# Optimization experiments

Measured on AMD Instinct MI355X. Metric: run time of the kernel, lower is better.

## Reference

```python
import jax, jax.numpy as jnp
import numpy as np

B, N, P = 8, 4096, 1024
P4 = P // 4
EPS = 1e-5


def _ln(x, g, b):
    mu = jnp.mean(x, axis=-1, keepdims=True)
    var = jnp.var(x, axis=-1, keepdims=True)
    return (x - mu) * jax.lax.rsqrt(var + EPS) * g + b


def setup_inputs() -> dict:
    key = jax.random.key(0)
    ks = jax.random.split(key, 16)
    s = lambda fan: 1.0 / np.sqrt(fan)
    return {
        "xyz": jax.random.normal(ks[0], (B, N, 3), jnp.float32),
        "x": jax.random.normal(ks[1], (B, N, P), jnp.float32),
        "ln1_g": jnp.ones((P,), jnp.float32),
        "ln1_b": jnp.zeros((P,), jnp.float32),
        "ln2_g": jnp.ones((P,), jnp.float32),
        "ln2_b": jnp.zeros((P,), jnp.float32),
        "qk_w": jax.random.normal(ks[2], (P4, P), jnp.float32) * s(P),   # shared q/k 1x1 conv, no bias
        "v_w": jax.random.normal(ks[3], (P, P), jnp.float32) * s(P),
        "v_b": jax.random.normal(ks[4], (P,), jnp.float32) * s(P),
        "t1_w": jax.random.normal(ks[5], (P, P4), jnp.float32) * s(P4),  # trans_conv
        "t1_b": jax.random.normal(ks[6], (P,), jnp.float32) * s(P4),
        "t2_w": jax.random.normal(ks[7], (P, P4), jnp.float32) * s(P4),  # trans_conv1
        "t2_b": jax.random.normal(ks[8], (P,), jnp.float32) * s(P4),
        "m1_w": jax.random.normal(ks[9], (P, P), jnp.float32) * s(P),
        "m1_b": jax.random.normal(ks[10], (P,), jnp.float32) * s(P),
        "m2_w": jax.random.normal(ks[11], (P, P), jnp.float32) * s(P),
        "m2_b": jax.random.normal(ks[12], (P,), jnp.float32) * s(P),
    }


def reference(xyz, x, ln1_g, ln1_b, ln2_g, ln2_b, qk_w, v_w, v_b,
              t1_w, t1_b, t2_w, t2_b, m1_w, m1_b, m2_w, m2_b):
    # xyz is accepted but unused, matching the torch module. Dropout = eval identity.
    res1 = x
    h = _ln(x, ln1_g, ln1_b)                                   # [B,N,P]
    # TransformerBlock_1 (1x1 convs on h^T [B,P,N] are just matmuls over P)
    x_q = jnp.einsum('op,bnp->bon', qk_w, h)                   # [B,P4,N]
    # k shares weights with q; x_k permuted is x_q transposed
    x_v = jnp.einsum('op,bnp->bno', v_w, h) + v_b              # [B,N,P]
    energy = jnp.einsum('bqn,bkn->bqk', x_q, x_q)              # [B,P4,P4]
    att = jnp.einsum('op,bpk->bok', t1_w, energy) + t1_b[:, None]   # [B,P,P4]
    att = jax.nn.gelu(att, approximate=False)
    att = jnp.einsum('op,bkp->bok', t2_w, att) + t2_b[:, None]      # [B,P,P]
    att = jax.nn.softmax(att, axis=-1)
    t_out = jnp.einsum('bnp,bpq->bnq', x_v, att)               # [B,N,P]
    x1 = t_out + res1
    h2 = _ln(x1, ln2_g, ln2_b)
    m = jax.nn.gelu(h2 @ m1_w.T + m1_b, approximate=False)
    m = m @ m2_w.T + m2_b
    return x1 + m
```

## Files before the change

kernel.cpp:

```cpp
#include <hip/hip_runtime.h>


typedef __attribute__((ext_vector_type(4))) float f32x4;
typedef __attribute__((ext_vector_type(8))) _Float16 h16x8;
typedef __attribute__((ext_vector_type(8))) unsigned short u16x8;
typedef __attribute__((ext_vector_type(4))) unsigned short u16x4;

__device__ __forceinline__ unsigned short f2h(float f) {
  _Float16 h = (_Float16)f;
  return __builtin_bit_cast(unsigned short, h);
}
__device__ __forceinline__ unsigned split16(float f) {
  _Float16 h = (_Float16)f;
  _Float16 l = (_Float16)(f - (float)h);
  return (unsigned)__builtin_bit_cast(unsigned short, h) |
         ((unsigned)__builtin_bit_cast(unsigned short, l) << 16);
}
__device__ __forceinline__ float gelu_f(float x) {
  return 0.5f * x * (1.0f + erff(x * 0.70710678118654752f));
}
__device__ __forceinline__ void gload16(const void* g, void* l) {
  __builtin_amdgcn_global_load_lds(
      (const __attribute__((address_space(1))) unsigned int*)g,
      (__attribute__((address_space(3))) unsigned int*)l, 16, 0, 0);
}
#define FENCE() asm volatile("" ::: "memory")

__global__ __launch_bounds__(256)
void ln_kernel(const float* __restrict__ x, const float* __restrict__ g,
               const float* __restrict__ b, unsigned short* __restrict__ hi,
               unsigned short* __restrict__ lo) {
  __shared__ float red[16];
  const size_t base = (size_t)blockIdx.x * 1024;
  const int t = threadIdx.x;
  f32x4 v = *(const f32x4*)&x[base + t * 4];
  float s = v[0] + v[1] + v[2] + v[3];
  float q = v[0] * v[0] + v[1] * v[1] + v[2] * v[2] + v[3] * v[3];
#pragma unroll
  for (int o = 32; o > 0; o >>= 1) { s += __shfl_down(s, o); q += __shfl_down(q, o); }
  const int w = t >> 6;
  if ((t & 63) == 0) { red[w] = s; red[8 + w] = q; }
  __syncthreads();
  s = (red[0] + red[1]) + (red[2] + red[3]);
  q = (red[8] + red[9]) + (red[10] + red[11]);
  const float mu = s * (1.0f / 1024.0f);
  const float var = q * (1.0f / 1024.0f) - mu * mu;
  const float is = rsqrtf(var + 1e-5f);
  f32x4 gg = *(const f32x4*)&g[t * 4];
  f32x4 bb = *(const f32x4*)&b[t * 4];
  u16x4 oh, ol;
#pragma unroll
  for (int j = 0; j < 4; j++) {
    float y = (v[j] - mu) * is * gg[j] + bb[j];
    unsigned p = split16(y);
    oh[j] = (unsigned short)(p & 0xffffu);
    ol[j] = (unsigned short)(p >> 16);
  }
  *(u16x4*)&hi[base + t * 4] = oh;
  if (lo) *(u16x4*)&lo[base + t * 4] = ol;
}

__global__ __launch_bounds__(256)
void cvt_kernel(const float* __restrict__ in, unsigned short* __restrict__ hi,
                unsigned short* __restrict__ lo, int n4) {
  int i = blockIdx.x * 256 + threadIdx.x;
  if (i < n4) {
    f32x4 v = *(const f32x4*)&in[(size_t)i * 4];
    u16x4 oh, ol;
#pragma unroll
    for (int j = 0; j < 4; j++) {
      unsigned p = split16(v[j]);
      oh[j] = (unsigned short)(p & 0xffffu);
      ol[j] = (unsigned short)(p >> 16);
    }
    *(u16x4*)&hi[(size_t)i * 4] = oh;
    if (lo) *(u16x4*)&lo[(size_t)i * 4] = ol;
  }
}

template <int EPI>
__global__ __launch_bounds__(512, 1)
void gemm_v(const unsigned short* __restrict__ Ain, const unsigned short* __restrict__ Bin,
            void* __restrict__ Cout, const float* __restrict__ bias,
            const float* __restrict__ resIn,
            int K, int lda, int ldb, int ldc,
            long long sA, long long sB, long long sC, long long sRes) {
  __shared__ short LDSall[65536];
  short* LA = LDSall;
  short* LB = LDSall + 32768;
  const int z = blockIdx.z;
  const unsigned short* A = Ain + (size_t)z * sA;
  const unsigned short* B = Bin + (size_t)z * sB;
  int bx = blockIdx.x, by = blockIdx.y;
  {
    const int nwg = gridDim.x * gridDim.y;
    if ((nwg & 7) == 0 && nwg >= 16) {
      const int flat = bx + gridDim.x * by;
      const int chunk = nwg >> 3;
      const int nf = (flat & 7) * chunk + (flat >> 3);
      bx = nf % gridDim.x;
      by = nf / gridDim.x;
    }
  }
  const int mBase = by * 256, nBase = bx * 256;
  const int t = threadIdx.x, w = t >> 6, l = t & 63;
  const int r16 = l & 15, kq = l >> 4;
  const int wr = (w >> 2) * 128, wc = (w & 3) * 64;
  f32x4 acc[8][4] = {};

  auto stage = [&](int buf, int k0) {
#pragma unroll
    for (int i = 0; i < 2; ++i) {
      const int c = i * 512 + t;
      const int row = c >> 2, cc = c & 3;
      const int gc = cc ^ ((row >> 1) & 3);
      const int cb = i * 512 + w * 64;
      gload16(&A[(size_t)(mBase + row) * lda + k0 + gc * 8], &LA[buf * 8192 + cb * 8]);
      gload16(&B[(size_t)(nBase + row) * ldb + k0 + gc * 8], &LB[buf * 8192 + cb * 8]);
    }
  };

  const int nt = K >> 5;
  stage(0, 0);
  stage(1, 32);
  stage(2, 64);
  for (int ts = 0; ts < nt; ++ts) {
    const int buf = ts & 3;
    if (ts + 3 <= nt) { asm volatile("s_waitcnt vmcnt(8)" ::: "memory"); }
    else if (ts + 2 == nt) { asm volatile("s_waitcnt vmcnt(4)" ::: "memory"); }
    else { asm volatile("s_waitcnt vmcnt(0)" ::: "memory"); }
    __builtin_amdgcn_s_barrier();
    FENCE();
    __builtin_amdgcn_s_setprio(1);
    {
      h16x8 aF[8], bF[4];
#pragma unroll
      for (int ni = 0; ni < 4; ni++) {
        const int r = wc + ni * 16 + r16;
        bF[ni] = *(const h16x8*)&LB[buf * 8192 + r * 32 + ((kq ^ ((r >> 1) & 3))) * 8];
      }
#pragma unroll
      for (int mi = 0; mi < 8; mi++) {
        const int r = wr + mi * 16 + r16;
        aF[mi] = *(const h16x8*)&LA[buf * 8192 + r * 32 + ((kq ^ ((r >> 1) & 3))) * 8];
      }
#pragma unroll
      for (int mi = 0; mi < 8; mi++)
#pragma unroll
        for (int ni = 0; ni < 4; ni++)
          acc[mi][ni] = __builtin_amdgcn_mfma_f32_16x16x32_f16(aF[mi], bF[ni], acc[mi][ni], 0, 0, 0);
    }
    __builtin_amdgcn_s_setprio(0);
    FENCE();
    __builtin_amdgcn_s_barrier();
    FENCE();
    if (ts + 3 < nt) stage((ts + 3) & 3, (ts + 3) * 32);
  }

  unsigned short* C16 = (unsigned short*)Cout + (size_t)z * sC;
  float* C32 = (float*)Cout + (size_t)z * sC;
  const float* res = (EPI >= 2) ? (resIn + (size_t)z * sRes) : nullptr;

  if constexpr (EPI <= 1) {
    short* ep = LDSall + w * 8192;
#pragma unroll
    for (int mi = 0; mi < 8; mi++) {
#pragma unroll
      for (int ni = 0; ni < 4; ni++) {
        const int cl = nBase + wc + ni * 16 + r16;
        const float bcol = bias[cl];
#pragma unroll
        for (int r = 0; r < 4; r++) {
          float v = acc[mi][ni][r] + bcol;
          if (EPI == 1) v = gelu_f(v);
          ep[(mi * 16 + kq * 4 + r) * 64 + ni * 16 + r16] = (short)f2h(v);
        }
      }
    }
#pragma unroll
    for (int j = 0; j < 16; j++) {
      const int f = j * 512 + l * 8;
      const int row = f >> 6, col = f & 63;
      u16x8 v8 = *(const u16x8*)&ep[f];
      *(u16x8*)&C16[(size_t)(mBase + wr + row) * ldc + nBase + wc + col] = v8;
    }
  } else {
#pragma unroll
    for (int mi = 0; mi < 8; mi++) {
#pragma unroll
      for (int ni = 0; ni < 4; ni++) {
        const int cl = nBase + wc + ni * 16 + r16;
        const float bcol = (EPI == 3) ? bias[cl] : 0.0f;
#pragma unroll
        for (int r = 0; r < 4; r++) {
          const int rw = mBase + wr + mi * 16 + kq * 4 + r;
          float v = acc[mi][ni][r] + bcol + res[(size_t)rw * ldc + cl];
          C32[(size_t)rw * ldc + cl] = v;
        }
      }
    }
  }
}

template <int EPI>
__global__ __launch_bounds__(256)
void gemm_s(const unsigned short* __restrict__ Ahi, const unsigned short* __restrict__ Alo,
            const unsigned short* __restrict__ Bhi, const unsigned short* __restrict__ Blo,
            void* __restrict__ Cout, unsigned short* __restrict__ Cout2,
            const float* __restrict__ bias,
            int K, int lda, int ldb, int ldc,
            long long sA, long long sB, long long sC, int splitK) {
  __shared__ short As[2][8192];
  __shared__ short Bs[2][8192];
  const int z = blockIdx.z;
  const int bi = z / splitK, sp = z % splitK;
  const int kLen = K / splitK, kStart = sp * kLen;
  const unsigned short* AH = Ahi + (size_t)bi * sA;
  const unsigned short* BH = Bhi + (size_t)bi * sB;
  const unsigned short* AL = Alo + (size_t)bi * sA;
  const unsigned short* BL = Blo + (size_t)bi * sB;
  int bx = blockIdx.x, by = blockIdx.y;
  {
    const int nwg = gridDim.x * gridDim.y;
    if ((nwg & 7) == 0 && nwg >= 16) {
      const int flat = bx + gridDim.x * by;
      const int chunk = nwg >> 3;
      const int nf = (flat & 7) * chunk + (flat >> 3);
      bx = nf % gridDim.x;
      by = nf / gridDim.x;
    }
  }
  const int mBase = by * 128, nBase = bx * 128;
  const int t = threadIdx.x, w = t >> 6, l = t & 63;
  const int r16 = l & 15, kq = l >> 4;
  const int wr = (w >> 1) * 64, wc = (w & 1) * 64;
  f32x4 acc[4][4] = {};

  auto stage = [&](int buf, int k0) {
#pragma unroll
    for (int i = 0; i < 2; ++i) {
      const int c = i * 256 + t;
      const int row = c >> 2, cc = c & 3;
      const int gc = cc ^ ((row >> 1) & 3);
      const int cbase = i * 256 + w * 64;
      const size_t ga = (size_t)(mBase + row) * lda + k0 + gc * 8;
      const size_t gb = (size_t)(nBase + row) * ldb + k0 + gc * 8;
      gload16(&AH[ga], &As[buf][cbase * 8]);
      gload16(&AL[ga], &As[buf][4096 + cbase * 8]);
      gload16(&BH[gb], &Bs[buf][cbase * 8]);
      gload16(&BL[gb], &Bs[buf][4096 + cbase * 8]);
    }
  };

  const int nsteps = kLen >> 5;
  stage(0, kStart);
  if (nsteps > 1) stage(1, kStart + 32);
  for (int ts = 0; ts < nsteps; ++ts) {
    const int cur = ts & 1;
    if (ts + 1 < nsteps) { asm volatile("s_waitcnt vmcnt(8)" ::: "memory"); }
    else                 { asm volatile("s_waitcnt vmcnt(0)" ::: "memory"); }
    __builtin_amdgcn_s_barrier();
    FENCE();
    h16x8 aH[4], bH[4], aL[4], bL[4];
#pragma unroll
    for (int mi = 0; mi < 4; mi++) {
      const int r = wr + mi * 16 + r16;
      const int off = r * 32 + (kq ^ ((r >> 1) & 3)) * 8;
      aH[mi] = *(const h16x8*)&As[cur][off];
      aL[mi] = *(const h16x8*)&As[cur][4096 + off];
    }
#pragma unroll
    for (int ni = 0; ni < 4; ni++) {
      const int r = wc + ni * 16 + r16;
      const int off = r * 32 + (kq ^ ((r >> 1) & 3)) * 8;
      bH[ni] = *(const h16x8*)&Bs[cur][off];
      bL[ni] = *(const h16x8*)&Bs[cur][4096 + off];
    }
    __builtin_amdgcn_s_setprio(1);
#pragma unroll
    for (int mi = 0; mi < 4; mi++)
#pragma unroll
      for (int ni = 0; ni < 4; ni++) {
        acc[mi][ni] = __builtin_amdgcn_mfma_f32_16x16x32_f16(aH[mi], bH[ni], acc[mi][ni], 0, 0, 0);
        acc[mi][ni] = __builtin_amdgcn_mfma_f32_16x16x32_f16(aH[mi], bL[ni], acc[mi][ni], 0, 0, 0);
        acc[mi][ni] = __builtin_amdgcn_mfma_f32_16x16x32_f16(aL[mi], bH[ni], acc[mi][ni], 0, 0, 0);
      }
    __builtin_amdgcn_s_setprio(0);
    FENCE();
    __builtin_amdgcn_s_barrier();
    FENCE();
    if (ts + 2 < nsteps) stage(cur, kStart + (ts + 2) * 32);
  }

  unsigned short* C16 = (unsigned short*)Cout + (size_t)z * sC;
  unsigned short* C16b = Cout2 ? Cout2 + (size_t)z * sC : nullptr;
  float* C32 = (float*)Cout + (size_t)z * sC;
#pragma unroll
  for (int mi = 0; mi < 4; mi++) {
#pragma unroll
    for (int ni = 0; ni < 4; ni++) {
      const int cl = nBase + wc + ni * 16 + r16;
#pragma unroll
      for (int r = 0; r < 4; r++) {
        const int rw = mBase + wr + mi * 16 + kq * 4 + r;
        float v = acc[mi][ni][r];
        if (EPI == 6 || EPI == 7) v += bias[rw];
        if (EPI == 6) v = gelu_f(v);
        const size_t idx = (size_t)rw * ldc + cl;
        if (EPI == 4 || EPI == 6) {
          unsigned p = split16(v);
          C16[idx] = (unsigned short)(p & 0xffffu);
          C16b[idx] = (unsigned short)(p >> 16);
        } else {
          C32[idx] = v;
        }
      }
    }
  }
}

__global__ __launch_bounds__(256)
void ereduce_kernel(const float* __restrict__ part, unsigned short* __restrict__ ehi,
                    unsigned short* __restrict__ elo) {
  const size_t idx = (size_t)blockIdx.x * 256 + threadIdx.x;
  const size_t b = idx >> 16, i = idx & 65535;
  const float* p = part + b * (8ull * 65536) + i;
  float s0 = (p[0] + p[65536]) + (p[2 * 65536] + p[3 * 65536]);
  float s1 = (p[4 * 65536] + p[5 * 65536]) + (p[6 * 65536] + p[7 * 65536]);
  unsigned pk = split16(s0 + s1);
  ehi[idx] = (unsigned short)(pk & 0xffffu);
  elo[idx] = (unsigned short)(pk >> 16);
}

__global__ __launch_bounds__(256)
void smax_t_kernel(const float* __restrict__ a2, unsigned short* __restrict__ attT) {
  __shared__ float S[8][1028];
  __shared__ float inv[8];
  const int t = threadIdx.x;
  const int b = blockIdx.y;
  const int o0 = blockIdx.x * 8;
  const float* src = a2 + ((size_t)b * 1024 + o0) * 1024;
#pragma unroll
  for (int i = 0; i < 8; i++)
    *(f32x4*)&S[i][t * 4] = *(const f32x4*)&src[(size_t)i * 1024 + t * 4];
  __syncthreads();
  const int w = t >> 6, l = t & 63;
  for (int rr = 0; rr < 2; rr++) {
    const int r = w * 2 + rr;
    float m = -1e30f;
#pragma unroll
    for (int i = 0; i < 16; i++) m = fmaxf(m, S[r][l + i * 64]);
#pragma unroll
    for (int o = 32; o > 0; o >>= 1) m = fmaxf(m, __shfl_xor(m, o));
    float ssum = 0.0f;
#pragma unroll
    for (int i = 0; i < 16; i++) {
      float e = expf(S[r][l + i * 64] - m);
      S[r][l + i * 64] = e;
      ssum += e;
    }
#pragma unroll
    for (int o = 32; o > 0; o >>= 1) ssum += __shfl_xor(ssum, o);
    if (l == 0) inv[r] = 1.0f / ssum;
  }
  __syncthreads();
  float iv[8];
#pragma unroll
  for (int r = 0; r < 8; r++) iv[r] = inv[r];
#pragma unroll
  for (int i = 0; i < 4; i++) {
    const int k = i * 256 + t;
    u16x8 ov;
#pragma unroll
    for (int r = 0; r < 8; r++) ov[r] = f2h(S[r][k] * iv[r]);
    *(u16x8*)&attT[((size_t)b * 1024 + k) * 1024 + o0] = ov;
  }
}

extern "C" void kernel_launch(void* const* d_in, const int* in_sizes, int n_in,
                              void* d_out, int out_size, void* d_ws, size_t ws_size,
                              hipStream_t stream) {
  (void)in_sizes; (void)n_in; (void)out_size; (void)ws_size;
  const float* x     = (const float*)d_in[1];
  const float* ln1_g = (const float*)d_in[2];
  const float* ln1_b = (const float*)d_in[3];
  const float* ln2_g = (const float*)d_in[4];
  const float* ln2_b = (const float*)d_in[5];
  const float* qk_w  = (const float*)d_in[6];
  const float* v_w   = (const float*)d_in[7];
  const float* v_b   = (const float*)d_in[8];
  const float* t1_w  = (const float*)d_in[9];
  const float* t1_b  = (const float*)d_in[10];
  const float* t2_w  = (const float*)d_in[11];
  const float* t2_b  = (const float*)d_in[12];
  const float* m1_w  = (const float*)d_in[13];
  const float* m1_b  = (const float*)d_in[14];
  const float* m2_w  = (const float*)d_in[15];
  const float* m2_b  = (const float*)d_in[16];

  char* ws = (char*)d_ws;
  unsigned short* hhi  = (unsigned short*)(ws + 0);
  unsigned short* hlo  = (unsigned short*)(ws + 67108864);
  unsigned short* Qthi = (unsigned short*)(ws + 134217728);
  unsigned short* Qtlo = (unsigned short*)(ws + 150994944);
  float*          part = (float*)(ws + 167772160);
  unsigned short* Ehi  = (unsigned short*)(ws + 184549376);
  unsigned short* Elo  = (unsigned short*)(ws + 185597952);
  unsigned short* Ghi  = (unsigned short*)(ws + 186646528);
  unsigned short* Glo  = (unsigned short*)(ws + 190840832);
  float*          a2   = (float*)(ws + 195035136);
  unsigned short* attT = (unsigned short*)(ws + 228589568);
  unsigned short* xv   = (unsigned short*)(ws + 245366784);
  float*          x1   = (float*)(ws + 312475648);
  unsigned short* wqh  = (unsigned short*)(ws + 446693376);
  unsigned short* wql  = (unsigned short*)(ws + 447217664);
  unsigned short* wv   = (unsigned short*)(ws + 447741952);
  unsigned short* wt1h = (unsigned short*)(ws + 449839104);
  unsigned short* wt1l = (unsigned short*)(ws + 450363392);
  unsigned short* wt2h = (unsigned short*)(ws + 450887680);
  unsigned short* wt2l = (unsigned short*)(ws + 451411968);
  unsigned short* wm1  = (unsigned short*)(ws + 451936256);
  unsigned short* wm2  = (unsigned short*)(ws + 454033408);
  unsigned short* h2 = hhi;
  unsigned short* gb = hlo;
  float* out = (float*)d_out;

  cvt_kernel<<<dim3(256),  dim3(256), 0, stream>>>(qk_w, wqh, wql, 65536);
  cvt_kernel<<<dim3(1024), dim3(256), 0, stream>>>(v_w, wv, nullptr, 262144);
  cvt_kernel<<<dim3(256),  dim3(256), 0, stream>>>(t1_w, wt1h, wt1l, 65536);
  cvt_kernel<<<dim3(256),  dim3(256), 0, stream>>>(t2_w, wt2h, wt2l, 65536);
  cvt_kernel<<<dim3(1024), dim3(256), 0, stream>>>(m1_w, wm1, nullptr, 262144);
  cvt_kernel<<<dim3(1024), dim3(256), 0, stream>>>(m2_w, wm2, nullptr, 262144);
  ln_kernel<<<dim3(32768), dim3(256), 0, stream>>>(x, ln1_g, ln1_b, hhi, hlo);
  gemm_s<4><<<dim3(32, 2, 8), dim3(256), 0, stream>>>(
      wqh, wql, hhi, hlo, Qthi, Qtlo, nullptr,
      1024, 1024, 1024, 4096, 0, 4194304, 1048576, 1);
  gemm_v<0><<<dim3(4, 128, 1), dim3(512), 0, stream>>>(
      hhi, wv, xv, v_b, nullptr, 1024, 1024, 1024, 1024, 0, 0, 0, 0);
  gemm_s<5><<<dim3(2, 2, 64), dim3(256), 0, stream>>>(
      Qthi, Qtlo, Qthi, Qtlo, part, nullptr, nullptr,
      4096, 4096, 4096, 256, 1048576, 1048576, 65536, 8);
  ereduce_kernel<<<dim3(2048), dim3(256), 0, stream>>>(part, Ehi, Elo);
  gemm_s<6><<<dim3(2, 8, 8), dim3(256), 0, stream>>>(
      wt1h, wt1l, Ehi, Elo, Ghi, Glo, t1_b,
      256, 256, 256, 256, 0, 65536, 262144, 1);
  gemm_s<7><<<dim3(8, 8, 8), dim3(256), 0, stream>>>(
      wt2h, wt2l, Ghi, Glo, a2, nullptr, t2_b,
      256, 256, 256, 1024, 0, 262144, 1048576, 1);
  smax_t_kernel<<<dim3(128, 8), dim3(256), 0, stream>>>(a2, attT);
  gemm_v<2><<<dim3(4, 16, 8), dim3(512), 0, stream>>>(
      xv, attT, x1, nullptr, x, 1024, 1024, 1024, 1024, 4194304, 1048576, 4194304, 4194304);
  ln_kernel<<<dim3(32768), dim3(256), 0, stream>>>(x1, ln2_g, ln2_b, h2, nullptr);
  gemm_v<1><<<dim3(4, 128, 1), dim3(512), 0, stream>>>(
      h2, wm1, gb, m1_b, nullptr, 1024, 1024, 1024, 1024, 0, 0, 0, 0);
  gemm_v<3><<<dim3(4, 128, 1), dim3(512), 0, stream>>>(
      gb, wm2, out, m2_b, x1, 1024, 1024, 1024, 1024, 0, 0, 0, 0);
}
```

Measured before the change: 712.9 us.

## Shrink GEMM tiles to 128x128, store x1 in fp16, add register-staged GEMM

The big fp16 GEMMs move from 256x256 tiles with 512 threads and a 4-stage LDS pipeline to 128x128 tiles with 256 threads and double buffering. The LDS-staged epilogue is replaced by direct scattered stores. The residual x1 is now stored as fp16 instead of fp32. A new register-staged GEMM produces it, and a new fp16-input layernorm reads it, cutting memory traffic for x1. The cost is lower per-tile data reuse, uncoalesced 2-byte epilogue stores, and reduced precision of the residual path.

```diff
diff --git a/kernel.cpp b/kernel.cpp
--- a/kernel.cpp
+++ b/kernel.cpp
@@ -2,6 +2,7 @@
 
 
 typedef __attribute__((ext_vector_type(4))) float f32x4;
+typedef __attribute__((ext_vector_type(4))) unsigned int u32x4;
 typedef __attribute__((ext_vector_type(8))) _Float16 h16x8;
 typedef __attribute__((ext_vector_type(8))) unsigned short u16x8;
 typedef __attribute__((ext_vector_type(4))) unsigned short u16x4;
@@ -9,6 +10,9 @@
 __device__ __forceinline__ unsigned short f2h(float f) {
   _Float16 h = (_Float16)f;
   return __builtin_bit_cast(unsigned short, h);
+}
+__device__ __forceinline__ float h2f(unsigned short u) {
+  return (float)__builtin_bit_cast(_Float16, u);
 }
 __device__ __forceinline__ unsigned split16(float f) {
   _Float16 h = (_Float16)f;
@@ -25,6 +29,17 @@
       (__attribute__((address_space(3))) unsigned int*)l, 16, 0, 0);
 }
 #define FENCE() asm volatile("" ::: "memory")
+
+__device__ __forceinline__ void xcd_swz(int& bx, int& by, int gx, int gy) {
+  const int nwg = gx * gy;
+  if ((nwg & 7) == 0 && nwg >= 16) {
+    const int flat = bx + gx * by;
+    const int chunk = nwg >> 3;
+    const int nf = (flat & 7) * chunk + (flat >> 3);
+    bx = nf % gx;
+    by = nf / gx;
+  }
+}
 
 __global__ __launch_bounds__(256)
 void ln_kernel(const float* __restrict__ x, const float* __restrict__ g,
@@ -61,6 +76,36 @@
 }
 
 __global__ __launch_bounds__(256)
+void ln16_kernel(const unsigned short* __restrict__ x16, const float* __restrict__ g,
+                 const float* __restrict__ b, unsigned short* __restrict__ hi) {
+  __shared__ float red[16];
+  const size_t base = (size_t)blockIdx.x * 1024;
+  const int t = threadIdx.x;
+  u16x4 raw = *(const u16x4*)&x16[base + t * 4];
+  float v[4];
+#pragma unroll
+  for (int j = 0; j < 4; j++) v[j] = h2f(raw[j]);
+  float s = v[0] + v[1] + v[2] + v[3];
+  float q = v[0] * v[0] + v[1] * v[1] + v[2] * v[2] + v[3] * v[3];
+#pragma unroll
+  for (int o = 32; o > 0; o >>= 1) { s += __shfl_down(s, o); q += __shfl_down(q, o); }
+  const int w = t >> 6;
+  if ((t & 63) == 0) { red[w] = s; red[8 + w] = q; }
+  __syncthreads();
+  s = (red[0] + red[1]) + (red[2] + red[3]);
+  q = (red[8] + red[9]) + (red[10] + red[11]);
+  const float mu = s * (1.0f / 1024.0f);
+  const float var = q * (1.0f / 1024.0f) - mu * mu;
+  const float is = rsqrtf(var + 1e-5f);
+  f32x4 gg = *(const f32x4*)&g[t * 4];
+  f32x4 bb = *(const f32x4*)&b[t * 4];
+  u16x4 oh;
+#pragma unroll
+  for (int j = 0; j < 4; j++) oh[j] = f2h((v[j] - mu) * is * gg[j] + bb[j]);
+  *(u16x4*)&hi[base + t * 4] = oh;
+}
+
+__global__ __launch_bounds__(256)
 void cvt_kernel(const float* __restrict__ in, unsigned short* __restrict__ hi,
                 unsigned short* __restrict__ lo, int n4) {
   int i = blockIdx.x * 256 + threadIdx.x;
@@ -79,124 +124,182 @@
 }
 
 template <int EPI>
-__global__ __launch_bounds__(512, 1)
+__global__ __launch_bounds__(256)
 void gemm_v(const unsigned short* __restrict__ Ain, const unsigned short* __restrict__ Bin,
             void* __restrict__ Cout, const float* __restrict__ bias,
-            const float* __restrict__ resIn,
+            const unsigned short* __restrict__ res16In,
             int K, int lda, int ldb, int ldc,
             long long sA, long long sB, long long sC, long long sRes) {
-  __shared__ short LDSall[65536];
-  short* LA = LDSall;
-  short* LB = LDSall + 32768;
+  __shared__ short As[2][4096];
+  __shared__ short Bs[2][4096];
   const int z = blockIdx.z;
   const unsigned short* A = Ain + (size_t)z * sA;
   const unsigned short* B = Bin + (size_t)z * sB;
   int bx = blockIdx.x, by = blockIdx.y;
-  {
-    const int nwg = gridDim.x * gridDim.y;
-    if ((nwg & 7) == 0 && nwg >= 16) {
-      const int flat = bx + gridDim.x * by;
-      const int chunk = nwg >> 3;
-      const int nf = (flat & 7) * chunk + (flat >> 3);
-      bx = nf % gridDim.x;
-      by = nf / gridDim.x;
-    }
-  }
-  const int mBase = by * 256, nBase = bx * 256;
+  xcd_swz(bx, by, gridDim.x, gridDim.y);
+  const int mBase = by * 128, nBase = bx * 128;
   const int t = threadIdx.x, w = t >> 6, l = t & 63;
   const int r16 = l & 15, kq = l >> 4;
-  const int wr = (w >> 2) * 128, wc = (w & 3) * 64;
-  f32x4 acc[8][4] = {};
+  const int wr = (w >> 1) * 64, wc = (w & 1) * 64;
+  f32x4 acc[4][4] = {};
 
   auto stage = [&](int buf, int k0) {
 #pragma unroll
     for (int i = 0; i < 2; ++i) {
-      const int c = i * 512 + t;
+      const int c = i * 256 + t;
       const int row = c >> 2, cc = c & 3;
       const int gc = cc ^ ((row >> 1) & 3);
-      const int cb = i * 512 + w * 64;
-      gload16(&A[(size_t)(mBase + row) * lda + k0 + gc * 8], &LA[buf * 8192 + cb * 8]);
-      gload16(&B[(size_t)(nBase + row) * ldb + k0 + gc * 8], &LB[buf * 8192 + cb * 8]);
+      short* la = &As[buf][(i * 256 + w * 64) * 8];
+      short* lb = &Bs[buf][(i * 256 + w * 64) * 8];
+      gload16(&A[(size_t)(mBase + row) * lda + k0 + gc * 8], la);
+      gload16(&B[(size_t)(nBase + row) * ldb + k0 + gc * 8], lb);
     }
   };
 
   const int nt = K >> 5;
   stage(0, 0);
-  stage(1, 32);
-  stage(2, 64);
+  if (nt > 1) stage(1, 32);
   for (int ts = 0; ts < nt; ++ts) {
-    const int buf = ts & 3;
-    if (ts + 3 <= nt) { asm volatile("s_waitcnt vmcnt(8)" ::: "memory"); }
-    else if (ts + 2 == nt) { asm volatile("s_waitcnt vmcnt(4)" ::: "memory"); }
-    else { asm volatile("s_waitcnt vmcnt(0)" ::: "memory"); }
+    const int cur = ts & 1;
+    if (ts + 1 < nt) { asm volatile("s_waitcnt vmcnt(4)" ::: "memory"); }
+    else             { asm volatile("s_waitcnt vmcnt(0)" ::: "memory"); }
     __builtin_amdgcn_s_barrier();
     FENCE();
+    h16x8 aF[4], bF[4];
+#pragma unroll
+    for (int mi = 0; mi < 4; mi++) {
+      const int r = wr + mi * 16 + r16;
+      aF[mi] = *(const h16x8*)&As[cur][r * 32 + (kq ^ ((r >> 1) & 3)) * 8];
+    }
+#pragma unroll
+    for (int ni = 0; ni < 4; ni++) {
+      const int r = wc + ni * 16 + r16;
+      bF[ni] = *(const h16x8*)&Bs[cur][r * 32 + (kq ^ ((r >> 1) & 3)) * 8];
+    }
     __builtin_amdgcn_s_setprio(1);
-    {
-      h16x8 aF[8], bF[4];
-#pragma unroll
-      for (int ni = 0; ni < 4; ni++) {
-        const int r = wc + ni * 16 + r16;
-        bF[ni] = *(const h16x8*)&LB[buf * 8192 + r * 32 + ((kq ^ ((r >> 1) & 3))) * 8];
-      }
-#pragma unroll
-      for (int mi = 0; mi < 8; mi++) {
-        const int r = wr + mi * 16 + r16;
-        aF[mi] = *(const h16x8*)&LA[buf * 8192 + r * 32 + ((kq ^ ((r >> 1) & 3))) * 8];
-      }
-#pragma unroll
-      for (int mi = 0; mi < 8; mi++)
-#pragma unroll
-        for (int ni = 0; ni < 4; ni++)
-          acc[mi][ni] = __builtin_amdgcn_mfma_f32_16x16x32_f16(aF[mi], bF[ni], acc[mi][ni], 0, 0, 0);
-    }
+#pragma unroll
+    for (int mi = 0; mi < 4; mi++)
+#pragma unroll
+      for (int ni = 0; ni < 4; ni++)
+        acc[mi][ni] = __builtin_amdgcn_mfma_f32_16x16x32_f16(aF[mi], bF[ni], acc[mi][ni], 0, 0, 0);
     __builtin_amdgcn_s_setprio(0);
     FENCE();
     __builtin_amdgcn_s_barrier();
     FENCE();
-    if (ts + 3 < nt) stage((ts + 3) & 3, (ts + 3) * 32);
+    if (ts + 2 < nt) stage(cur, (ts + 2) * 32);
   }
 
   unsigned short* C16 = (unsigned short*)Cout + (size_t)z * sC;
   float* C32 = (float*)Cout + (size_t)z * sC;
-  const float* res = (EPI >= 2) ? (resIn + (size_t)z * sRes) : nullptr;
-
-  if constexpr (EPI <= 1) {
-    short* ep = LDSall + w * 8192;
-#pragma unroll
-    for (int mi = 0; mi < 8; mi++) {
-#pragma unroll
-      for (int ni = 0; ni < 4; ni++) {
-        const int cl = nBase + wc + ni * 16 + r16;
-        const float bcol = bias[cl];
-#pragma unroll
-        for (int r = 0; r < 4; r++) {
-          float v = acc[mi][ni][r] + bcol;
-          if (EPI == 1) v = gelu_f(v);
-          ep[(mi * 16 + kq * 4 + r) * 64 + ni * 16 + r16] = (short)f2h(v);
-        }
+  const unsigned short* res16 = (EPI == 3) ? (res16In + (size_t)z * sRes) : nullptr;
+#pragma unroll
+  for (int mi = 0; mi < 4; mi++) {
+#pragma unroll
+    for (int ni = 0; ni < 4; ni++) {
+      const int cl = nBase + wc + ni * 16 + r16;
+      const float bcol = bias[cl];
+#pragma unroll
+      for (int r = 0; r < 4; r++) {
+        const int rw = mBase + wr + mi * 16 + kq * 4 + r;
+        float v = acc[mi][ni][r] + bcol;
+        if (EPI == 1) v = gelu_f(v);
+        const size_t idx = (size_t)rw * ldc + cl;
+        if (EPI == 3) { v += h2f(res16[idx]); C32[idx] = v; }
+        else          C16[idx] = f2h(v);
       }
     }
-#pragma unroll
-    for (int j = 0; j < 16; j++) {
-      const int f = j * 512 + l * 8;
-      const int row = f >> 6, col = f & 63;
-      u16x8 v8 = *(const u16x8*)&ep[f];
-      *(u16x8*)&C16[(size_t)(mBase + wr + row) * ldc + nBase + wc + col] = v8;
-    }
-  } else {
-#pragma unroll
-    for (int mi = 0; mi < 8; mi++) {
-#pragma unroll
-      for (int ni = 0; ni < 4; ni++) {
-        const int cl = nBase + wc + ni * 16 + r16;
-        const float bcol = (EPI == 3) ? bias[cl] : 0.0f;
-#pragma unroll
-        for (int r = 0; r < 4; r++) {
-          const int rw = mBase + wr + mi * 16 + kq * 4 + r;
-          float v = acc[mi][ni][r] + bcol + res[(size_t)rw * ldc + cl];
-          C32[(size_t)rw * ldc + cl] = v;
-        }
+  }
+}
+
+__global__ __launch_bounds__(256)
+void gemm_r(const unsigned short* __restrict__ Ain, const unsigned short* __restrict__ Bin,
+            unsigned short* __restrict__ Cout, const float* __restrict__ resIn,
+            int K, int lda, int ldb, int ldc,
+            long long sA, long long sB, long long sC, long long sRes) {
+  __shared__ short As[2][4096];
+  __shared__ short Bs[2][4096];
+  const int z = blockIdx.z;
+  const unsigned short* A = Ain + (size_t)z * sA;
+  const unsigned short* B = Bin + (size_t)z * sB;
+  int bx = blockIdx.x, by = blockIdx.y;
+  xcd_swz(bx, by, gridDim.x, gridDim.y);
+  const int mBase = by * 128, nBase = bx * 128;
+  const int t = threadIdx.x, w = t >> 6, l = t & 63;
+  const int r16 = l & 15, kq = l >> 4;
+  const int wr = (w >> 1) * 64, wc = (w & 1) * 64;
+  f32x4 acc[4][4] = {};
+
+  u32x4 ra0, ra1, rb0, rb1;
+  auto loadreg = [&](int k0) {
+#pragma unroll
+    for (int i = 0; i < 2; ++i) {
+      const int c = i * 256 + t;
+      const int row = c >> 2, cc = c & 3;
+      const int gc = cc ^ ((row >> 1) & 3);
+      u32x4 va = *(const u32x4*)&A[(size_t)(mBase + row) * lda + k0 + gc * 8];
+      u32x4 vb = *(const u32x4*)&B[(size_t)(nBase + row) * ldb + k0 + gc * 8];
+      if (i == 0) { ra0 = va; rb0 = vb; } else { ra1 = va; rb1 = vb; }
+    }
+  };
+  auto dswrite = [&](int buf) {
+    *(u32x4*)&As[buf][t * 8] = ra0;
+    *(u32x4*)&Bs[buf][t * 8] = rb0;
+    *(u32x4*)&As[buf][(256 + t) * 8] = ra1;
+    *(u32x4*)&Bs[buf][(256 + t) * 8] = rb1;
+  };
+
+  const int nt = K >> 5;
+  loadreg(0);
+  dswrite(0);
+  if (nt > 1) loadreg(32);
+  asm volatile("s_waitcnt lgkmcnt(0)" ::: "memory");
+  __builtin_amdgcn_s_barrier();
+  FENCE();
+  for (int ts = 0; ts < nt; ++ts) {
+    const int cur = ts & 1;
+    h16x8 aF[4], bF[4];
+#pragma unroll
+    for (int mi = 0; mi < 4; mi++) {
+      const int r = wr + mi * 16 + r16;
+      aF[mi] = *(const h16x8*)&As[cur][r * 32 + (kq ^ ((r >> 1) & 3)) * 8];
+    }
+#pragma unroll
+    for (int ni = 0; ni < 4; ni++) {
+      const int r = wc + ni * 16 + r16;
+      bF[ni] = *(const h16x8*)&Bs[cur][r * 32 + (kq ^ ((r >> 1) & 3)) * 8];
+    }
+    __builtin_amdgcn_s_setprio(1);
+#pragma unroll
+    for (int mi = 0; mi < 4; mi++)
+#pragma unroll
+      for (int ni = 0; ni < 4; ni++)
+        acc[mi][ni] = __builtin_amdgcn_mfma_f32_16x16x32_f16(aF[mi], bF[ni], acc[mi][ni], 0, 0, 0);
+    __builtin_amdgcn_s_setprio(0);
+    FENCE();
+    if (ts + 1 < nt) {
+      __builtin_amdgcn_s_barrier();
+      FENCE();
+      dswrite((ts + 1) & 1);
+      if (ts + 2 < nt) loadreg((ts + 2) * 32);
+      asm volatile("s_waitcnt lgkmcnt(0)" ::: "memory");
+      FENCE();
+      __builtin_amdgcn_s_barrier();
+      FENCE();
+    }
+  }
+
+  unsigned short* C16 = Cout + (size_t)z * sC;
+  const float* res = resIn + (size_t)z * sRes;
+#pragma unroll
+  for (int mi = 0; mi < 4; mi++) {
+#pragma unroll
+    for (int ni = 0; ni < 4; ni++) {
+      const int cl = nBase + wc + ni * 16 + r16;
+#pragma unroll
+      for (int r = 0; r < 4; r++) {
+        const int rw = mBase + wr + mi * 16 + kq * 4 + r;
+        const size_t idx = (size_t)rw * ldc + cl;
+        C16[idx] = f2h(acc[mi][ni][r] + res[idx]);
       }
     }
   }
@@ -220,16 +323,7 @@
   const unsigned short* AL = Alo + (size_t)bi * sA;
   const unsigned short* BL = Blo + (size_t)bi * sB;
   int bx = blockIdx.x, by = blockIdx.y;
-  {
-    const int nwg = gridDim.x * gridDim.y;
-    if ((nwg & 7) == 0 && nwg >= 16) {
-      const int flat = bx + gridDim.x * by;
-      const int chunk = nwg >> 3;
-      const int nf = (flat & 7) * chunk + (flat >> 3);
-      bx = nf % gridDim.x;
-      by = nf / gridDim.x;
-    }
-  }
+  xcd_swz(bx, by, gridDim.x, gridDim.y);
   const int mBase = by * 128, nBase = bx * 128;
   const int t = threadIdx.x, w = t >> 6, l = t & 63;
   const int r16 = l & 15, kq = l >> 4;
@@ -411,7 +505,7 @@
   float*          a2   = (float*)(ws + 195035136);
   unsigned short* attT = (unsigned short*)(ws + 228589568);
   unsigned short* xv   = (unsigned short*)(ws + 245366784);
-  float*          x1   = (float*)(ws + 312475648);
+  unsigned short* x1h  = (unsigned short*)(ws + 312475648);
   unsigned short* wqh  = (unsigned short*)(ws + 446693376);
   unsigned short* wql  = (unsigned short*)(ws + 447217664);
   unsigned short* wv   = (unsigned short*)(ws + 447741952);
@@ -435,7 +529,7 @@
   gemm_s<4><<<dim3(32, 2, 8), dim3(256), 0, stream>>>(
       wqh, wql, hhi, hlo, Qthi, Qtlo, nullptr,
       1024, 1024, 1024, 4096, 0, 4194304, 1048576, 1);
-  gemm_v<0><<<dim3(4, 128, 1), dim3(512), 0, stream>>>(
+  gemm_v<0><<<dim3(8, 256, 1), dim3(256), 0, stream>>>(
       hhi, wv, xv, v_b, nullptr, 1024, 1024, 1024, 1024, 0, 0, 0, 0);
   gemm_s<5><<<dim3(2, 2, 64), dim3(256), 0, stream>>>(
       Qthi, Qtlo, Qthi, Qtlo, part, nullptr, nullptr,
@@ -448,11 +542,11 @@
       wt2h, wt2l, Ghi, Glo, a2, nullptr, t2_b,
       256, 256, 256, 1024, 0, 262144, 1048576, 1);
   smax_t_kernel<<<dim3(128, 8), dim3(256), 0, stream>>>(a2, attT);
-  gemm_v<2><<<dim3(4, 16, 8), dim3(512), 0, stream>>>(
-      xv, attT, x1, nullptr, x, 1024, 1024, 1024, 1024, 4194304, 1048576, 4194304, 4194304);
-  ln_kernel<<<dim3(32768), dim3(256), 0, stream>>>(x1, ln2_g, ln2_b, h2, nullptr);
-  gemm_v<1><<<dim3(4, 128, 1), dim3(512), 0, stream>>>(
+  gemm_r<<<dim3(8, 32, 8), dim3(256), 0, stream>>>(
+      xv, attT, x1h, x, 1024, 1024, 1024, 1024, 4194304, 1048576, 4194304, 4194304);
+  ln16_kernel<<<dim3(32768), dim3(256), 0, stream>>>(x1h, ln2_g, ln2_b, h2);
+  gemm_v<1><<<dim3(8, 256, 1), dim3(256), 0, stream>>>(
       h2, wm1, gb, m1_b, nullptr, 1024, 1024, 1024, 1024, 0, 0, 0, 0);
-  gemm_v<3><<<dim3(4, 128, 1), dim3(512), 0, stream>>>(
-      gb, wm2, out, m2_b, x1, 1024, 1024, 1024, 1024, 0, 0, 0, 0);
-}
+  gemm_v<3><<<dim3(8, 256, 1), dim3(256), 0, stream>>>(
+      gb, wm2, out, m2_b, x1h, 1024, 1024, 1024, 1024, 0, 0, 0, 0);
+}
```

Result: no change. 714.1 us (+0.2%).
